# Optimization experiments

Measured on AMD Instinct MI355X. Metric: run time of the kernel, lower is better.

Reference implementation:

```python
import jax, jax.numpy as jnp
import numpy as np

TAU = 0.2
K = 15  # k_neighbors


def setup_inputs() -> dict:
    key = jax.random.key(0)
    k1, k2 = jax.random.split(key)
    Nx, Ny, C = 16384, 16384, 128
    feat_x = jax.random.normal(k1, (Nx, C), dtype=jnp.float32)
    feat_y = jax.random.normal(k2, (Ny, C), dtype=jnp.float32)
    return {"feat_x": feat_x, "feat_y": feat_y}


def reference(feat_x, feat_y):
    # similarity: [Nx, Ny] = (feat_x @ feat_y^T) / tau  (torch chunks this for
    # memory; math is identical computed in one shot)
    sim = jnp.matmul(feat_x, feat_y.T) / TAU
    # top-k per row (torch uses sorted=False; set membership is identical)
    topk_vals, topk_idx = jax.lax.top_k(sim, K)          # [Nx, K] each
    # softmax over the k selected values per row
    topk_softmax = jax.nn.softmax(topk_vals, axis=1)     # [Nx, K]
    # sparse COO equivalent: row r has nonzeros at cols topk_idx[r, :] with
    # values topk_softmax[r, :] in an (Nx, Ny) matrix.
    return topk_softmax, topk_idx
```

## Files before the change

kernel.cpp:

```cpp
#include <hip/hip_runtime.h>
#include <math.h>

#define NX 16384
#define NY 16384
#define CD 128
#define KSEL 15
#define CAP 192
#define WCAP 640
#define ZTH 2.6601f
#define INV_TAU 5.0f
#define GATE_DELTA 0.06f

typedef unsigned short u16;
typedef unsigned long long u64;
typedef __attribute__((ext_vector_type(8))) short bf16x8;
typedef __attribute__((ext_vector_type(4))) float f32x4;

__device__ __forceinline__ u16 f2bf(float f) {
    unsigned u = __float_as_uint(f);
    return (u16)((u + 0x7FFF + ((u >> 16) & 1)) >> 16);
}

__global__ __launch_bounds__(256) void prep_xy(const float* __restrict__ X,
                                               const float* __restrict__ Y,
                                               u16* __restrict__ Xt,
                                               u16* __restrict__ Yt,
                                               int* __restrict__ cnt) {
    const int t = threadIdx.x;
    if (blockIdx.x < NX / 4) {
        const int w = t >> 6, l = t & 63;
        const int row = blockIdx.x * 4 + w;
        if (l == 0) cnt[row] = 0;
        float2 xv = *(const float2*)&X[(size_t)row * CD + 2 * l];
        float s = xv.x * xv.x + xv.y * xv.y;
        #pragma unroll
        for (int off = 32; off; off >>= 1) s += __shfl_xor(s, off);
        float inv = 1.0f / sqrtf(s);
        unsigned pk = (unsigned)f2bf(xv.x * inv) | ((unsigned)f2bf(xv.y * inv) << 16);
        int src = (l & 15) * 4;
        unsigned g0 = __shfl(pk, src + 0);
        unsigned g1 = __shfl(pk, src + 1);
        unsigned g2 = __shfl(pk, src + 2);
        unsigned g3 = __shfl(pk, src + 3);
        if (l < 16) {
            int4 chunk = make_int4(g0, g1, g2, g3);
            *(int4*)&Xt[((size_t)l * NX + row) * 8] = chunk;
        }
    } else {
        const int bid = blockIdx.x - NX / 4;
        const int col = bid * 16 + (t & 15);
        const int kq = t >> 4;
        const float* y = Y + (size_t)col * CD + kq * 8;
        float4 a = *(const float4*)y;
        float4 b = *(const float4*)(y + 4);
        u16 ch[8] = {f2bf(a.x), f2bf(a.y), f2bf(a.z), f2bf(a.w),
                     f2bf(b.x), f2bf(b.y), f2bf(b.z), f2bf(b.w)};
        *(int4*)&Yt[((size_t)kq * NY + col) * 8] = *(int4*)ch;
    }
}

__global__ __launch_bounds__(256, 3) void pass_a(const u16* __restrict__ Xt,
                                                 const u16* __restrict__ Yt,
                                                 int* __restrict__ cnt,
                                                 int* __restrict__ cand) {
    __shared__ int2 plist[4][WCAP];
    __shared__ int pcnt[4];
    const int t = threadIdx.x;
    const int w = t >> 6, l = t & 63;
    const int quad = l >> 4, lo = l & 15;
    const int wrow = w >> 1, wc = w & 1;
    const int b = blockIdx.x;
    const int cq = b & 7;
    const int rg = b >> 3;
    const int rowbase = rg * 128;
    const int colw0 = cq * 2048 + wc * 1024;

    if (l == 0) pcnt[w] = 0;

    bf16x8 afr[4][4];
    #pragma unroll
    for (int s = 0; s < 4; s++)
        #pragma unroll
        for (int rt = 0; rt < 4; rt++) {
            const u16* ap = &Xt[((size_t)(s * 4 + quad) * NX +
                                 rowbase + wrow * 64 + rt * 16 + lo) * 8];
            asm volatile("global_load_dwordx4 %0, %1, off"
                         : "=&v"(afr[rt][s]) : "v"(ap));
        }

    const u64 yb0 = (u64)Yt;
    const u64 yb1 = yb0 + ((u64)4 * NY * 16);
    const u64 yb2 = yb0 + ((u64)8 * NY * 16);
    const u64 yb3 = yb0 + ((u64)12 * NY * 16);
    unsigned voff = ((unsigned)quad * NY + (unsigned)(colw0 + lo)) * 16u;

    bf16x8 bA[4], bB[4];
    asm volatile("global_load_dwordx4 %0, %8, %4\n\t"
                 "global_load_dwordx4 %1, %8, %5\n\t"
                 "global_load_dwordx4 %2, %8, %6\n\t"
                 "global_load_dwordx4 %3, %8, %7"
                 : "=&v"(bA[0]), "=&v"(bA[1]), "=&v"(bA[2]), "=&v"(bA[3])
                 : "s"(yb0), "s"(yb1), "s"(yb2), "s"(yb3), "v"(voff));
    voff += 256;
    asm volatile("global_load_dwordx4 %0, %8, %4\n\t"
                 "global_load_dwordx4 %1, %8, %5\n\t"
                 "global_load_dwordx4 %2, %8, %6\n\t"
                 "global_load_dwordx4 %3, %8, %7"
                 : "=&v"(bB[0]), "=&v"(bB[1]), "=&v"(bB[2]), "=&v"(bB[3])
                 : "s"(yb0), "s"(yb1), "s"(yb2), "s"(yb3), "v"(voff));
    voff += 256;

    asm volatile("s_waitcnt vmcnt(8)"
                 : "+v"(afr[0][0]), "+v"(afr[0][1]), "+v"(afr[0][2]), "+v"(afr[0][3]),
                   "+v"(afr[1][0]), "+v"(afr[1][1]), "+v"(afr[1][2]), "+v"(afr[1][3]),
                   "+v"(afr[2][0]), "+v"(afr[2][1]), "+v"(afr[2][2]), "+v"(afr[2][3]),
                   "+v"(afr[3][0]), "+v"(afr[3][1]), "+v"(afr[3][2]), "+v"(afr[3][3])
                 :: "memory");

    const f32x4 zero = {0.f, 0.f, 0.f, 0.f};
    int pc0 = (((wrow * 64 + quad * 4) << 14) | lo) + colw0;

    #define STEP_BODY(BCUR)                                                     \
    do {                                                                        \
        asm volatile("s_waitcnt vmcnt(4)"                                       \
                     : "+v"(BCUR[0]), "+v"(BCUR[1]),                            \
                       "+v"(BCUR[2]), "+v"(BCUR[3]) :: "memory");               \
        f32x4 acc[4];                                                           \
        _Pragma("unroll")                                                       \
        for (int rt = 0; rt < 4; rt++)                                          \
            acc[rt] = __builtin_amdgcn_mfma_f32_16x16x32_bf16(                  \
                afr[rt][0], BCUR[0], zero, 0, 0, 0);                            \
        _Pragma("unroll")                                                       \
        for (int s = 1; s < 4; s++)                                             \
            _Pragma("unroll")                                                   \
            for (int rt = 0; rt < 4; rt++)                                      \
                acc[rt] = __builtin_amdgcn_mfma_f32_16x16x32_bf16(              \
                    afr[rt][s], BCUR[s], acc[rt], 0, 0, 0);                     \
        asm volatile("global_load_dwordx4 %0, %8, %4\n\t"                       \
                     "global_load_dwordx4 %1, %8, %5\n\t"                       \
                     "global_load_dwordx4 %2, %8, %6\n\t"                       \
                     "global_load_dwordx4 %3, %8, %7"                           \
                     : "=&v"(BCUR[0]), "=&v"(BCUR[1]),                          \
                       "=&v"(BCUR[2]), "=&v"(BCUR[3])                           \
                     : "s"(yb0), "s"(yb1), "s"(yb2), "s"(yb3), "v"(voff));      \
        voff += 256;                                                            \
        _Pragma("unroll")                                                       \
        for (int rt = 0; rt < 4; rt++) {                                        \
            float m01 = fmaxf(acc[rt][0], acc[rt][1]);                          \
            float m23 = fmaxf(acc[rt][2], acc[rt][3]);                          \
            if (fmaxf(m01, m23) > ZTH) {                                        \
                _Pragma("unroll")                                               \
                for (int r = 0; r < 4; r++) {                                   \
                    float v = acc[rt][r];                                       \
                    if (v > ZTH) {                                              \
                        int packed = pc0 + ((rt * 16 + r) << 14);               \
                        int slot = atomicAdd(&pcnt[w], 1);                      \
                        if (slot < WCAP) {                                      \
                            plist[w][slot] = make_int2(packed,                  \
                                                       __float_as_int(v));      \
                        } else {                                                \
                            int row = rowbase + (packed >> 14);                 \
                            unsigned q = (__float_as_uint(v) >> 13) & 0x3FFFFu; \
                            int s2 = atomicAdd(&cnt[row], 1);                   \
                            if (s2 < CAP)                                       \
                                cand[row * CAP + s2] =                          \
                                    (int)((q << 14) |                           \
                                          (unsigned)(packed & 0x3FFF));         \
                            asm volatile("s_waitcnt vmcnt(0)" ::: "memory");    \
                        }                                                       \
                    }                                                           \
                }                                                               \
            }                                                                   \
        }                                                                       \
        pc0 += 16;                                                              \
    } while (0)

    for (int stp = 0; stp < 32; stp++) {
        STEP_BODY(bA);
        STEP_BODY(bB);
    }
    #undef STEP_BODY

    asm volatile("s_waitcnt vmcnt(0)" ::: "memory");

    int total = pcnt[w];
    if (total > WCAP) total = WCAP;
    for (int i = l; i < total; i += 64) {
        int2 e = plist[w][i];
        int row = rowbase + (e.x >> 14);
        unsigned q = ((unsigned)e.y >> 13) & 0x3FFFFu;
        int s2 = atomicAdd(&cnt[row], 1);
        if (s2 < CAP) cand[row * CAP + s2] = (int)((q << 14) | (unsigned)(e.x & 0x3FFF));
    }
}

__global__ __launch_bounds__(256) void refine(const float* __restrict__ X,
                                              const float* __restrict__ Y,
                                              const int* __restrict__ cnt,
                                              const int* __restrict__ cand,
                                              float* __restrict__ out) {
    __shared__ float xs[4][CD];
    const int w = threadIdx.x >> 6, l = threadIdx.x & 63;
    const int row = blockIdx.x * 4 + w;

    float2 xv = *(const float2*)&X[(size_t)row * CD + 2 * l];
    xs[w][2 * l] = xv.x;
    xs[w][2 * l + 1] = xv.y;
    __syncthreads();

    const float* xr = xs[w];
    int c = cnt[row];
    if (c > CAP) c = CAP;
    const int base = row * CAP;

    auto dotf = [&](int col) {
        const float* y = Y + (size_t)col * CD;
        float a = 0.f;
        #pragma unroll 8
        for (int k = 0; k < CD; k += 4) {
            float4 yv = *(const float4*)&y[k];
            a = fmaf(xr[k], yv.x, a);
            a = fmaf(xr[k + 1], yv.y, a);
            a = fmaf(xr[k + 2], yv.z, a);
            a = fmaf(xr[k + 3], yv.w, a);
        }
        return a;
    };

    unsigned p0 = (l < c) ? (unsigned)cand[base + l] : 0u;
    unsigned p1 = (64 + l < c) ? (unsigned)cand[base + 64 + l] : 0u;
    unsigned p2 = (128 + l < c) ? (unsigned)cand[base + 128 + l] : 0u;
    unsigned q0 = p0 >> 14, q1 = p1 >> 14, q2 = p2 >> 14;

    unsigned pref = 0;
    for (int bit = 17; bit >= 0; bit--) {
        unsigned tq = pref | (1u << bit);
        int cc = __popcll(__ballot(q0 >= tq)) +
                 __popcll(__ballot(q1 >= tq)) +
                 __popcll(__ballot(q2 >= tq));
        if (cc >= KSEL) pref = tq;
    }
    const float thresh = __uint_as_float(pref << 13) - GATE_DELTA;

    u64 k0 = 0, k1 = 0, k2 = 0;
    if (p0 && __uint_as_float(q0 << 13) >= thresh) {
        int cc = (int)(p0 & 0x3FFFu);
        k0 = ((u64)__float_as_uint(dotf(cc)) << 32) | (unsigned)(~cc);
    }
    if (p1 && __uint_as_float(q1 << 13) >= thresh) {
        int cc = (int)(p1 & 0x3FFFu);
        k1 = ((u64)__float_as_uint(dotf(cc)) << 32) | (unsigned)(~cc);
    }
    if (p2 && __uint_as_float(q2 << 13) >= thresh) {
        int cc = (int)(p2 & 0x3FFFu);
        k2 = ((u64)__float_as_uint(dotf(cc)) << 32) | (unsigned)(~cc);
    }

    float wv[KSEL];
    int wi[KSEL];
    for (int r = 0; r < KSEL; r++) {
        u64 bk = k0 > k1 ? k0 : k1;
        if (k2 > bk) bk = k2;
        #pragma unroll
        for (int off = 1; off < 64; off <<= 1) {
            u64 ok = __shfl_xor(bk, off);
            if (ok > bk) bk = ok;
        }
        wv[r] = __uint_as_float((unsigned)(bk >> 32));
        wi[r] = (int)(~(unsigned)bk);
        bool m0 = (k0 == bk), m1 = (k1 == bk), m2 = (k2 == bk);
        u64 ball = __ballot(m0 || m1 || m2);
        int owner = (int)__ffsll((long long)ball) - 1;
        if (l == owner) {
            if (m0)      k0 = 0;
            else if (m1) k1 = 0;
            else         k2 = 0;
        }
    }

    if (l < KSEL) {
        float mx = wv[0] * INV_TAU;
        float s = 0.f;
        #pragma unroll
        for (int i = 0; i < KSEL; i++) s += __expf(wv[i] * INV_TAU - mx);
        float e = __expf(wv[l] * INV_TAU - mx);
        out[(size_t)row * KSEL + l] = e / s;
        out[(size_t)NX * KSEL + (size_t)row * KSEL + l] = (float)wi[l];
    }
}

extern "C" void kernel_launch(void* const* d_in, const int* in_sizes, int n_in,
                              void* d_out, int out_size, void* d_ws, size_t ws_size,
                              hipStream_t stream) {
    const float* feat_x = (const float*)d_in[0];
    const float* feat_y = (const float*)d_in[1];
    float* out = (float*)d_out;

    char* ws = (char*)d_ws;
    u16* Yt   = (u16*)(ws);
    u16* Xt   = (u16*)(ws + (size_t)4 * 1024 * 1024);
    int* cnt  = (int*)(ws + (size_t)8 * 1024 * 1024);
    int* cand = (int*)(ws + (size_t)8 * 1024 * 1024 + 65536);

    prep_xy<<<NX / 4 + NY / 16, 256, 0, stream>>>(feat_x, feat_y, Xt, Yt, cnt);
    pass_a<<<1024, 256, 0, stream>>>(Xt, Yt, cnt, cand);
    refine<<<NX / 4, 256, 0, stream>>>(feat_x, feat_y, cnt, cand, out);
}
```

Before: 200.8 us.

## Share Y tiles across waves via LDS direct loads in pass_a

The candidate-filter GEMM pass now stages each Y column tile into a 4-deep LDS ring with global_load_lds, and all four waves read the same tile from LDS instead of each loading its own B fragments from global memory. Block tiling changes from 128 rows by 2048 columns split across waves to 256 rows by 1024 columns, with every wave covering the full column range for its own 64 rows. This is meant to cut global/L2 traffic for Y by sharing it across waves. In exchange it adds a workgroup barrier and an LDS read wait on every step, which can stall waves that hit the threshold-append path.

```diff
diff --git a/kernel.cpp b/kernel.cpp
--- a/kernel.cpp
+++ b/kernel.cpp
@@ -15,6 +15,8 @@
 typedef unsigned long long u64;
 typedef __attribute__((ext_vector_type(8))) short bf16x8;
 typedef __attribute__((ext_vector_type(4))) float f32x4;
+typedef __attribute__((address_space(1))) const unsigned gu32;
+typedef __attribute__((address_space(3))) unsigned lu32;
 
 __device__ __forceinline__ u16 f2bf(float f) {
     unsigned u = __float_as_uint(f);
@@ -63,17 +65,15 @@
                                                  const u16* __restrict__ Yt,
                                                  int* __restrict__ cnt,
                                                  int* __restrict__ cand) {
+    __shared__ __align__(16) u16 Bt[4][2048];
     __shared__ int2 plist[4][WCAP];
     __shared__ int pcnt[4];
     const int t = threadIdx.x;
     const int w = t >> 6, l = t & 63;
     const int quad = l >> 4, lo = l & 15;
-    const int wrow = w >> 1, wc = w & 1;
     const int b = blockIdx.x;
-    const int cq = b & 7;
-    const int rg = b >> 3;
-    const int rowbase = rg * 128;
-    const int colw0 = cq * 2048 + wc * 1024;
+    const int colbase = (b & 15) * 1024;
+    const int rowbase = (b >> 4) * 256;
 
     if (l == 0) pcnt[w] = 0;
 
@@ -83,34 +83,24 @@
         #pragma unroll
         for (int rt = 0; rt < 4; rt++) {
             const u16* ap = &Xt[((size_t)(s * 4 + quad) * NX +
-                                 rowbase + wrow * 64 + rt * 16 + lo) * 8];
+                                 rowbase + w * 64 + rt * 16 + lo) * 8];
             asm volatile("global_load_dwordx4 %0, %1, off"
                          : "=&v"(afr[rt][s]) : "v"(ap));
         }
 
-    const u64 yb0 = (u64)Yt;
-    const u64 yb1 = yb0 + ((u64)4 * NY * 16);
-    const u64 yb2 = yb0 + ((u64)8 * NY * 16);
-    const u64 yb3 = yb0 + ((u64)12 * NY * 16);
-    unsigned voff = ((unsigned)quad * NY + (unsigned)(colw0 + lo)) * 16u;
-
-    bf16x8 bA[4], bB[4];
-    asm volatile("global_load_dwordx4 %0, %8, %4\n\t"
-                 "global_load_dwordx4 %1, %8, %5\n\t"
-                 "global_load_dwordx4 %2, %8, %6\n\t"
-                 "global_load_dwordx4 %3, %8, %7"
-                 : "=&v"(bA[0]), "=&v"(bA[1]), "=&v"(bA[2]), "=&v"(bA[3])
-                 : "s"(yb0), "s"(yb1), "s"(yb2), "s"(yb3), "v"(voff));
-    voff += 256;
-    asm volatile("global_load_dwordx4 %0, %8, %4\n\t"
-                 "global_load_dwordx4 %1, %8, %5\n\t"
-                 "global_load_dwordx4 %2, %8, %6\n\t"
-                 "global_load_dwordx4 %3, %8, %7"
-                 : "=&v"(bB[0]), "=&v"(bB[1]), "=&v"(bB[2]), "=&v"(bB[3])
-                 : "s"(yb0), "s"(yb1), "s"(yb2), "s"(yb3), "v"(voff));
-    voff += 256;
-
-    asm volatile("s_waitcnt vmcnt(8)"
+    const u16* gsrc = &Yt[((size_t)(w * 4 + quad) * NY + colbase + lo) * 8];
+    lu32* ldsdst0 = (lu32*)&Bt[0][w * 512];
+    lu32* ldsdst1 = (lu32*)&Bt[1][w * 512];
+    lu32* ldsdst2 = (lu32*)&Bt[2][w * 512];
+    lu32* ldsdst3 = (lu32*)&Bt[3][w * 512];
+    lu32* rbase = (lu32*)&Bt[0][(quad * 16 + lo) * 8];
+
+    __builtin_amdgcn_global_load_lds((gu32*)gsrc, ldsdst0, 16, 0, 0);
+    gsrc += 128;
+    __builtin_amdgcn_global_load_lds((gu32*)gsrc, ldsdst1, 16, 0, 0);
+    gsrc += 128;
+
+    asm volatile("s_waitcnt vmcnt(2)"
                  : "+v"(afr[0][0]), "+v"(afr[0][1]), "+v"(afr[0][2]), "+v"(afr[0][3]),
                    "+v"(afr[1][0]), "+v"(afr[1][1]), "+v"(afr[1][2]), "+v"(afr[1][3]),
                    "+v"(afr[2][0]), "+v"(afr[2][1]), "+v"(afr[2][2]), "+v"(afr[2][3]),
@@ -118,32 +108,42 @@
                  :: "memory");
 
     const f32x4 zero = {0.f, 0.f, 0.f, 0.f};
-    int pc0 = (((wrow * 64 + quad * 4) << 14) | lo) + colw0;
-
-    #define STEP_BODY(BCUR)                                                     \
+    int pc0 = (((w * 64 + quad * 4) << 14) | lo) + colbase;
+
+    #define DSR(dst, off)                                                       \
+        asm volatile("ds_read_b128 %0, %1 offset:%c2"                           \
+                     : "=v"(dst) : "v"(rbase), "i"(off))
+
+    #define STEP(RS, WS)                                                        \
     do {                                                                        \
-        asm volatile("s_waitcnt vmcnt(4)"                                       \
-                     : "+v"(BCUR[0]), "+v"(BCUR[1]),                            \
-                       "+v"(BCUR[2]), "+v"(BCUR[3]) :: "memory");               \
+        asm volatile("s_waitcnt vmcnt(1)" ::: "memory");                        \
+        __builtin_amdgcn_s_barrier();                                           \
+        __builtin_amdgcn_global_load_lds((gu32*)gsrc, ldsdst##WS, 16, 0, 0);    \
+        gsrc += 128;                                                            \
+        bf16x8 b0, b1, b2, b3;                                                  \
+        DSR(b0, (RS) * 4096 + 0);                                               \
+        DSR(b1, (RS) * 4096 + 1024);                                            \
+        DSR(b2, (RS) * 4096 + 2048);                                            \
+        DSR(b3, (RS) * 4096 + 3072);                                            \
+        asm volatile("s_waitcnt lgkmcnt(0)"                                     \
+                     : "+v"(b0), "+v"(b1), "+v"(b2), "+v"(b3) :: "memory");     \
         f32x4 acc[4];                                                           \
         _Pragma("unroll")                                                       \
         for (int rt = 0; rt < 4; rt++)                                          \
             acc[rt] = __builtin_amdgcn_mfma_f32_16x16x32_bf16(                  \
-                afr[rt][0], BCUR[0], zero, 0, 0, 0);                            \
-        _Pragma("unroll")                                                       \
-        for (int s = 1; s < 4; s++)                                             \
-            _Pragma("unroll")                                                   \
-            for (int rt = 0; rt < 4; rt++)                                      \
-                acc[rt] = __builtin_amdgcn_mfma_f32_16x16x32_bf16(              \
-                    afr[rt][s], BCUR[s], acc[rt], 0, 0, 0);                     \
-        asm volatile("global_load_dwordx4 %0, %8, %4\n\t"                       \
-                     "global_load_dwordx4 %1, %8, %5\n\t"                       \
-                     "global_load_dwordx4 %2, %8, %6\n\t"                       \
-                     "global_load_dwordx4 %3, %8, %7"                           \
-                     : "=&v"(BCUR[0]), "=&v"(BCUR[1]),                          \
-                       "=&v"(BCUR[2]), "=&v"(BCUR[3])                           \
-                     : "s"(yb0), "s"(yb1), "s"(yb2), "s"(yb3), "v"(voff));      \
-        voff += 256;                                                            \
+                afr[rt][0], b0, zero, 0, 0, 0);                                 \
+        _Pragma("unroll")                                                       \
+        for (int rt = 0; rt < 4; rt++)                                          \
+            acc[rt] = __builtin_amdgcn_mfma_f32_16x16x32_bf16(                  \
+                afr[rt][1], b1, acc[rt], 0, 0, 0);                              \
+        _Pragma("unroll")                                                       \
+        for (int rt = 0; rt < 4; rt++)                                          \
+            acc[rt] = __builtin_amdgcn_mfma_f32_16x16x32_bf16(                  \
+                afr[rt][2], b2, acc[rt], 0, 0, 0);                              \
+        _Pragma("unroll")                                                       \
+        for (int rt = 0; rt < 4; rt++)                                          \
+            acc[rt] = __builtin_amdgcn_mfma_f32_16x16x32_bf16(                  \
+                afr[rt][3], b3, acc[rt], 0, 0, 0);                              \
         _Pragma("unroll")                                                       \
         for (int rt = 0; rt < 4; rt++) {                                        \
             float m01 = fmaxf(acc[rt][0], acc[rt][1]);                          \
@@ -175,11 +175,14 @@
         pc0 += 16;                                                              \
     } while (0)
 
-    for (int stp = 0; stp < 32; stp++) {
-        STEP_BODY(bA);
-        STEP_BODY(bB);
-    }
-    #undef STEP_BODY
+    for (int i = 0; i < 16; i++) {
+        STEP(0, 2);
+        STEP(1, 3);
+        STEP(2, 0);
+        STEP(3, 1);
+    }
+    #undef STEP
+    #undef DSR
 
     asm volatile("s_waitcnt vmcnt(0)" ::: "memory");
 
```

New measurement: 213.1 us. +6.2%, slower.
